# Optimization experiments

Hardware: AMD Instinct MI355X
Metric: run time of the kernel (lower is better)

The kernel has to match this reference:

```python
import jax, jax.numpy as jnp
import numpy as np

IMG = 32
CX = CY = IMG // 2
B = 65536


def setup_inputs() -> dict:
    key = jax.random.key(0)
    k1, k2, k3 = jax.random.split(key, 3)
    W = jax.random.normal(k1, (B, 16), dtype=jnp.float32)
    noise_randn = jax.random.normal(k2, (B, IMG, IMG), dtype=jnp.float32)
    noise_rand = jax.random.uniform(k3, (B, IMG, IMG), dtype=jnp.float32)
    return {"W": W, "noise_randn": noise_randn, "noise_rand": noise_rand}


def reference(W, noise_randn, noise_rand):
    H = IMG
    PI = jnp.float32(np.pi)
    ar = jnp.arange(H, dtype=jnp.float32)
    xx, yy = jnp.meshgrid(ar, ar, indexing="ij")  # (H, H)

    def c(k):  # per-sample scalar broadcast to (B,1,1)
        return W[:, k][:, None, None]

    r = jnp.sqrt((xx - CX) ** 2 + (yy - CY) ** 2)  # (H, H)

    # layer 0: clipped radial cone
    img = jnp.clip(c(0) * 5 - r, 0.0, 1.0)
    # layer 1: centered square (torch int(clamp(...).item()) == floor for positive vals)
    half = jnp.floor(jnp.clip(jnp.abs(c(1)) * 8, 2.0, 12.0))
    mask1 = ((xx >= CY - half) & (xx < CY + half) & (yy >= CX - half) & (yy < CX + half))
    img = img + 0.5 * mask1.astype(jnp.float32)
    # layers 2-4: sinusoids
    img = img + 0.5 * jnp.sin(c(2) * 10 * PI * xx / H)
    img = img + 0.5 * jnp.sin(c(3) * 10 * PI * yy / H)
    img = img + 0.5 * jnp.sin(c(4) * 5 * PI * (xx + yy) / (2 * H))
    # layer 5: warp
    img = img + 0.5 * jnp.sin((yy + c(5) * 10) * PI / H)
    # layer 6: bias
    img = img + c(6)
    # layer 7: gaussian blob; int() truncates toward zero
    bx = jnp.trunc(CX + c(7) * 5)
    by = jnp.trunc(CY + c(7) * 5)
    sigma = 4.0 + jnp.abs(c(7)) * 4.0
    img = img + jnp.exp(-((xx - bx) ** 2 + (yy - by) ** 2) / (2 * sigma ** 2))
    # layer 8: ring
    img = img + ((r - c(8) * 10) ** 2 < 10.0).astype(jnp.float32)
    # layer 9: checkerboard; cb_size = int(clamp(|w|*8+2, 2, 16)) -> floor
    cb = jnp.floor(jnp.clip(jnp.abs(c(9)) * 8 + 2, 2.0, 16.0))
    img = img + jnp.mod(jnp.floor(xx / cb) + jnp.floor(yy / cb), 2.0) * 0.3
    # layer 10: rotated line
    angle = c(10) * PI
    rot_line = jnp.cos(angle) * (xx - CX) + jnp.sin(angle) * (yy - CY)
    img = img + (jnp.abs(rot_line) < 3.0).astype(jnp.float32) * 0.6
    # layer 11: angular sinusoid
    theta = jnp.arctan2(yy - CY, xx - CX)
    img = img + 0.5 * jnp.sin(theta * c(11) * 5)
    # layers 12-13: noise (deterministic inputs replace randn_like/rand_like)
    img = img + noise_randn * 0.1 * c(12)
    img = img + (noise_rand - 0.5) * c(13) * 0.05
    # layer 14: contrast
    img = (img - 0.5) * (1.0 + c(14)) + 0.5
    # layer 15: conditional inversion
    img = jnp.where(c(15) > 0, 1.0 - img, img)
    # per-image min-max normalize
    mn = jnp.min(img, axis=(1, 2), keepdims=True)
    mx = jnp.max(img, axis=(1, 2), keepdims=True)
    img = (img - mn) / (mx - mn + 1e-8)
    return img[:, None, :, :]  # (B, 1, H, W)
```

## Files before the change

### kernel.cpp

```cpp
#include <hip/hip_runtime.h>
#include <math.h>

#define NB 65536
#define IMGD 32
#define NPIX 1024
#define PSTRIDE 20

__device__ float g_r[NPIX];
__device__ float g_th[NPIX];
__device__ float g_par[(size_t)NB * PSTRIDE];

__global__ void init_params_kernel(const float* __restrict__ W) {
    int b = blockIdx.x * blockDim.x + threadIdx.x;

    if (blockIdx.x == 0) {
        int t = threadIdx.x;
        for (int k = 0; k < 4; ++k) {
            int p = t * 4 + k;
            int x = p >> 5, y = p & 31;
            float dx = (float)(x - 16), dy = (float)(y - 16);
            g_r[p] = sqrtf(dx * dx + dy * dy);
            g_th[p] = atan2f(dy, dx) * 0.79577471545947668f;
        }
    }
    if (b >= NB) return;
    const float* w = W + (size_t)b * 16;
    float* P = g_par + (size_t)b * PSTRIDE;

    float w0 = w[0], w1 = w[1], w2 = w[2], w3 = w[3], w4 = w[4], w5 = w[5],
          w6 = w[6], w7 = w[7], w8 = w[8], w9 = w[9], w10 = w[10], w11 = w[11],
          w12 = w[12], w13 = w[13], w14 = w[14], w15 = w[15];

    P[0] = w0 * 5.0f;
    float half = floorf(fminf(fmaxf(fabsf(w1) * 8.0f, 2.0f), 12.0f));
    P[1] = 16.0f - half;
    P[2] = 16.0f + half;
    P[3] = w2 * 0.15625f;
    P[4] = w3 * 0.15625f;
    P[5] = w4 * 0.0390625f;
    P[6] = w5 * 0.15625f;
    P[7] = w6;
    float t7 = __fadd_rn(16.0f, __fmul_rn(w7, 5.0f));
    P[8] = truncf(t7);
    float sg = 4.0f + fabsf(w7) * 4.0f;
    P[9] = -1.0f / (2.0f * sg * sg);
    P[10] = w8 * 10.0f;
    float cb = floorf(fminf(fmaxf(__fadd_rn(fabsf(w9) * 8.0f, 2.0f), 2.0f), 16.0f));
    P[11] = cb;
    P[12] = 1.0f / cb;
    float ang = __fmul_rn(w10, 3.14159265358979323846f);
    P[13] = (float)cos((double)ang);
    P[14] = (float)sin((double)ang);
    P[15] = w11;
    P[16] = w12 * 0.1f;
    P[17] = w13 * 0.05f;
    P[18] = 1.0f + w14;
    P[19] = w15;
}

__device__ __forceinline__ float hsin(float rev) {
    rev = rev - floorf(rev);
    return __builtin_amdgcn_sinf(rev);
}

__device__ __forceinline__ float fdivq(float xf, float cb, float rcb) {
    float q = floorf(xf * rcb);
    q += ((q + 1.0f) * cb <= xf) ? 1.0f : 0.0f;
    q -= ((q * cb) > xf) ? 1.0f : 0.0f;
    return q;
}

__global__ __launch_bounds__(256) void decode_kernel(
        const float* __restrict__ nrand,
        const float* __restrict__ nunif,
        float* __restrict__ out) {
    int b = blockIdx.x;
    int t = threadIdx.x;
    const float* P = g_par + (size_t)b * PSTRIDE;

    float a0  = P[0],  lo  = P[1],  hi  = P[2],  s2  = P[3],  s3 = P[4];
    float s4  = P[5],  s5o = P[6],  w6  = P[7],  bxy = P[8],  nk = P[9];
    float t8  = P[10], cb  = P[11], rcb = P[12], ca  = P[13], sa = P[14];
    float w11 = P[15], k12 = P[16], k13 = P[17], con = P[18], w15 = P[19];

    __shared__ float4 xt4[32];
    __shared__ float4 yt4[36];
    __shared__ float  stab[63];

    if (t < 32) {
        float xf = (float)t;
        float qx = fdivq(xf, cb, rcb);
        float px = qx - 2.0f * floorf(qx * 0.5f);
        float d  = xf - bxy;
        float4 e;
        e.x = 0.5f * hsin(s2 * xf) + 0.3f * px;
        e.y = (xf >= lo && xf < hi) ? 1.0f : 0.0f;
        e.z = -0.6f * px;
        e.w = __expf(d * d * nk);
        xt4[t] = e;
    } else if (t < 64) {
        int   y  = t - 32;
        float yf = (float)y;
        float qy = fdivq(yf, cb, rcb);
        float py = qy - 2.0f * floorf(qy * 0.5f);
        float d  = yf - bxy;
        float4 e;
        e.x = 0.5f * hsin(s3 * yf) + 0.5f * hsin(0.015625f * yf + s5o)
              + 0.3f * py + w6;
        e.y = (yf >= lo && yf < hi) ? 0.5f : 0.0f;
        e.z = py;
        e.w = __expf(d * d * nk);
        yt4[y + (y >> 3)] = e;
    } else if (t < 127) {
        int s = t - 64;
        stab[s] = 0.5f * hsin(s4 * (float)s);
    }
    __syncthreads();

    int   y   = t & 31;
    int   x0  = t >> 5;
    float4 Y  = yt4[y + (y >> 3)];
    float yf  = (float)y;
    float sy  = __fmul_rn(sa, yf - 16.0f);

    size_t base = (size_t)b * NPIX + (size_t)t;
    const float* nrp = nrand + base;
    const float* nup = nunif + base;
    const float* rp  = g_r + t;
    const float* tp  = g_th + t;

    float img[4];
    float mn = 1e30f, mx = -1e30f;

#pragma unroll
    for (int j = 0; j < 4; ++j) {
        int   x  = x0 + 8 * j;
        float xf = (float)x;
        float r  = rp[256 * j];
        float4 X = xt4[x];

        float v = fminf(fmaxf(a0 - r, 0.0f), 1.0f);
        v += X.x + Y.x;
        v = fmaf(X.y, Y.y, v);
        v += stab[x + y];
        v = fmaf(X.z, Y.z, v);
        v = fmaf(X.w, Y.w, v);
        float dr = __fsub_rn(r, t8);
        v += (__fmul_rn(dr, dr) < 10.0f) ? 1.0f : 0.0f;
        float rot = __fadd_rn(__fmul_rn(ca, xf - 16.0f), sy);
        v += (fabsf(rot) < 3.0f) ? 0.6f : 0.0f;
        v += 0.5f * hsin(tp[256 * j] * w11);
        v = fmaf(nrp[256 * j], k12, v);
        v = fmaf(nup[256 * j] - 0.5f, k13, v);

        img[j] = v;
        mn = fminf(mn, v);
        mx = fmaxf(mx, v);
    }

#pragma unroll
    for (int off = 32; off > 0; off >>= 1) {
        mn = fminf(mn, __shfl_xor(mn, off));
        mx = fmaxf(mx, __shfl_xor(mx, off));
    }
    __shared__ float smn[4], smx[4];
    int wid = t >> 6;
    if ((t & 63) == 0) { smn[wid] = mn; smx[wid] = mx; }
    __syncthreads();
    mn = fminf(fminf(smn[0], smn[1]), fminf(smn[2], smn[3]));
    mx = fmaxf(fmaxf(smx[0], smx[1]), fmaxf(smx[2], smx[3]));

    float ac    = fabsf(con);
    float denom = fmaf(ac, mx - mn, 1e-8f);
    float s     = ac / denom;
    bool  eff   = (w15 > 0.0f) != (con < 0.0f);
    float bse   = eff ? mx : mn;
    float sgn   = eff ? -s : s;

    float* op = out + base;
#pragma unroll
    for (int j = 0; j < 4; ++j)
        op[256 * j] = (img[j] - bse) * sgn;
}

extern "C" void kernel_launch(void* const* d_in, const int* in_sizes, int n_in,
                              void* d_out, int out_size, void* d_ws, size_t ws_size,
                              hipStream_t stream) {
    const float* W  = (const float*)d_in[0];
    const float* nr = (const float*)d_in[1];
    const float* nu = (const float*)d_in[2];
    float* out = (float*)d_out;

    init_params_kernel<<<NB / 256, 256, 0, stream>>>(W);
    decode_kernel<<<NB, 256, 0, stream>>>(nr, nu, out);
}
```

Measured before the change: 147.2 us.

## Vectorize pixel loads/stores to float4 and pack math with v_pk_fma_f32

```diff
diff --git a/kernel.cpp b/kernel.cpp
--- a/kernel.cpp
+++ b/kernel.cpp
@@ -6,9 +6,24 @@
 #define NPIX 1024
 #define PSTRIDE 20
 
-__device__ float g_r[NPIX];
-__device__ float g_th[NPIX];
-__device__ float g_par[(size_t)NB * PSTRIDE];
+typedef float v2f __attribute__((ext_vector_type(2)));
+
+#define PK_FMA(d, a, b, c) \
+    asm("v_pk_fma_f32 %0, %1, %2, %3" : "=v"(d) : "v"(a), "v"(b), "v"(c))
+#define PK_FMA_CLAMP(d, a, b, c) \
+    asm("v_pk_fma_f32 %0, %1, %2, %3 clamp" : "=v"(d) : "v"(a), "v"(b), "v"(c))
+#define PK_FMA_ACC(acc, a, b) \
+    asm("v_pk_fma_f32 %0, %1, %2, %0" : "+v"(acc) : "v"(a), "v"(b))
+#define PK_ADD(d, a, b) \
+    asm("v_pk_add_f32 %0, %1, %2" : "=v"(d) : "v"(a), "v"(b))
+#define PK_ADD_ACC(acc, a) \
+    asm("v_pk_add_f32 %0, %0, %1" : "+v"(acc) : "v"(a))
+#define PK_MUL(d, a, b) \
+    asm("v_pk_mul_f32 %0, %1, %2" : "=v"(d) : "v"(a), "v"(b))
+
+__device__ __align__(16) float g_r[NPIX];
+__device__ __align__(16) float g_th[NPIX];
+__device__ __align__(16) float g_par[(size_t)NB * PSTRIDE];
 
 __global__ void init_params_kernel(const float* __restrict__ W) {
     int b = blockIdx.x * blockDim.x + threadIdx.x;
@@ -59,8 +74,7 @@
 }
 
 __device__ __forceinline__ float hsin(float rev) {
-    rev = rev - floorf(rev);
-    return __builtin_amdgcn_sinf(rev);
+    return __builtin_amdgcn_sinf(__builtin_amdgcn_fractf(rev));
 }
 
 __device__ __forceinline__ float fdivq(float xf, float cb, float rcb) {
@@ -76,15 +90,22 @@
         float* __restrict__ out) {
     int b = blockIdx.x;
     int t = threadIdx.x;
-    const float* P = g_par + (size_t)b * PSTRIDE;
-
-    float a0  = P[0],  lo  = P[1],  hi  = P[2],  s2  = P[3],  s3 = P[4];
-    float s4  = P[5],  s5o = P[6],  w6  = P[7],  bxy = P[8],  nk = P[9];
-    float t8  = P[10], cb  = P[11], rcb = P[12], ca  = P[13], sa = P[14];
-    float w11 = P[15], k12 = P[16], k13 = P[17], con = P[18], w15 = P[19];
+
+    const float4* Pq = (const float4*)(g_par + (size_t)b * PSTRIDE);
+    float4 q0 = Pq[0], q1 = Pq[1], q2 = Pq[2], q3 = Pq[3], q4 = Pq[4];
+    float a0 = q0.x, lo = q0.y, hi = q0.z, s2 = q0.w;
+    float s3 = q1.x, s4 = q1.y, s5o = q1.z, w6 = q1.w;
+    float bxy = q2.x, nk = q2.y, t8 = q2.z, cb = q2.w;
+    float rcb = q3.x, ca = q3.y, sa = q3.z, w11 = q3.w;
+    float k12 = q4.x, k13 = q4.y, con = q4.z, w15 = q4.w;
 
     __shared__ float4 xt4[32];
-    __shared__ float4 yt4[36];
+    __shared__ float  rx[32];
+    __shared__ float  ysum[32];
+    __shared__ float  ym05[32];
+    __shared__ float  pyt[32];
+    __shared__ float  gyt[32];
+    __shared__ float  syt[32];
     __shared__ float  stab[63];
 
     if (t < 32) {
@@ -98,64 +119,97 @@
         e.z = -0.6f * px;
         e.w = __expf(d * d * nk);
         xt4[t] = e;
+        rx[t] = __fmul_rn(ca, xf - 16.0f);
     } else if (t < 64) {
         int   y  = t - 32;
         float yf = (float)y;
         float qy = fdivq(yf, cb, rcb);
         float py = qy - 2.0f * floorf(qy * 0.5f);
         float d  = yf - bxy;
-        float4 e;
-        e.x = 0.5f * hsin(s3 * yf) + 0.5f * hsin(0.015625f * yf + s5o)
-              + 0.3f * py + w6;
-        e.y = (yf >= lo && yf < hi) ? 0.5f : 0.0f;
-        e.z = py;
-        e.w = __expf(d * d * nk);
-        yt4[y + (y >> 3)] = e;
+        ysum[y] = 0.5f * hsin(s3 * yf) + 0.5f * hsin(0.015625f * yf + s5o)
+                  + 0.3f * py + w6 - 0.5f * k13;
+        ym05[y] = (yf >= lo && yf < hi) ? 0.5f : 0.0f;
+        pyt[y]  = py;
+        gyt[y]  = __expf(d * d * nk);
+        syt[y]  = __fmul_rn(sa, yf - 16.0f);
     } else if (t < 127) {
         int s = t - 64;
         stab[s] = 0.5f * hsin(s4 * (float)s);
     }
     __syncthreads();
 
-    int   y   = t & 31;
-    int   x0  = t >> 5;
-    float4 Y  = yt4[y + (y >> 3)];
-    float yf  = (float)y;
-    float sy  = __fmul_rn(sa, yf - 16.0f);
-
-    size_t base = (size_t)b * NPIX + (size_t)t;
-    const float* nrp = nrand + base;
-    const float* nup = nunif + base;
-    const float* rp  = g_r + t;
-    const float* tp  = g_th + t;
-
-    float img[4];
-    float mn = 1e30f, mx = -1e30f;
+    int x  = t >> 3;
+    int y0 = (t & 7) * 4;
+
+    float4 X   = xt4[x];
+    float  rxv = rx[x];
+
+    v2f ysA = *(const v2f*)&ysum[y0], ysB = *(const v2f*)&ysum[y0 + 2];
+    v2f ymA = *(const v2f*)&ym05[y0], ymB = *(const v2f*)&ym05[y0 + 2];
+    v2f pyA = *(const v2f*)&pyt[y0],  pyB = *(const v2f*)&pyt[y0 + 2];
+    v2f gyA = *(const v2f*)&gyt[y0],  gyB = *(const v2f*)&gyt[y0 + 2];
+    v2f syA = *(const v2f*)&syt[y0],  syB = *(const v2f*)&syt[y0 + 2];
+    int s0 = x + y0;
+    v2f stA = {stab[s0], stab[s0 + 1]}, stB = {stab[s0 + 2], stab[s0 + 3]};
+
+    size_t q = (size_t)b * 256 + (size_t)t;
+    float4 R  = ((const float4*)g_r)[t];
+    float4 TH = ((const float4*)g_th)[t];
+    float4 NR = ((const float4*)nrand)[q];
+    float4 NU = ((const float4*)nunif)[q];
+
+    const v2f m1   = {-1.0f, -1.0f};
+    const v2f a02  = {a0, a0};
+    const v2f xs2  = {X.x, X.x};
+    const v2f xm2  = {X.y, X.y};
+    const v2f px2  = {X.z, X.z};
+    const v2f gx2  = {X.w, X.w};
+    const v2f rx2  = {rxv, rxv};
+    const v2f nt82 = {-t8, -t8};
+    const v2f w112 = {w11, w11};
+    const v2f h2   = {0.5f, 0.5f};
+    const v2f k122 = {k12, k12};
+    const v2f k132 = {k13, k13};
+
+    v2f i01, i23;
+    float mn, mx;
 
 #pragma unroll
-    for (int j = 0; j < 4; ++j) {
-        int   x  = x0 + 8 * j;
-        float xf = (float)x;
-        float r  = rp[256 * j];
-        float4 X = xt4[x];
-
-        float v = fminf(fmaxf(a0 - r, 0.0f), 1.0f);
-        v += X.x + Y.x;
-        v = fmaf(X.y, Y.y, v);
-        v += stab[x + y];
-        v = fmaf(X.z, Y.z, v);
-        v = fmaf(X.w, Y.w, v);
-        float dr = __fsub_rn(r, t8);
-        v += (__fmul_rn(dr, dr) < 10.0f) ? 1.0f : 0.0f;
-        float rot = __fadd_rn(__fmul_rn(ca, xf - 16.0f), sy);
-        v += (fabsf(rot) < 3.0f) ? 0.6f : 0.0f;
-        v += 0.5f * hsin(tp[256 * j] * w11);
-        v = fmaf(nrp[256 * j], k12, v);
-        v = fmaf(nup[256 * j] - 0.5f, k13, v);
-
-        img[j] = v;
-        mn = fminf(mn, v);
-        mx = fmaxf(mx, v);
+    for (int k = 0; k < 2; ++k) {
+        v2f r2  = k ? (v2f){R.z, R.w}   : (v2f){R.x, R.y};
+        v2f th2 = k ? (v2f){TH.z, TH.w} : (v2f){TH.x, TH.y};
+        v2f nr2 = k ? (v2f){NR.z, NR.w} : (v2f){NR.x, NR.y};
+        v2f nu2 = k ? (v2f){NU.z, NU.w} : (v2f){NU.x, NU.y};
+        v2f ys = k ? ysB : ysA, ym = k ? ymB : ymA, py = k ? pyB : pyA;
+        v2f gy = k ? gyB : gyA, sy = k ? syB : syA, st = k ? stB : stA;
+
+        v2f v;
+        PK_FMA_CLAMP(v, r2, m1, a02);
+        PK_ADD_ACC(v, ys);
+        PK_ADD_ACC(v, xs2);
+        PK_ADD_ACC(v, st);
+        PK_FMA_ACC(v, xm2, ym);
+        PK_FMA_ACC(v, px2, py);
+        PK_FMA_ACC(v, gx2, gy);
+        v2f dr, dr2, rot, ang;
+        PK_ADD(dr, r2, nt82);
+        PK_MUL(dr2, dr, dr);
+        PK_ADD(rot, sy, rx2);
+        PK_MUL(ang, th2, w112);
+        v2f sn = {hsin(ang.x), hsin(ang.y)};
+        PK_FMA_ACC(v, sn, h2);
+        PK_FMA_ACC(v, nr2, k122);
+        PK_FMA_ACC(v, nu2, k132);
+
+        float vx = v.x + ((dr2.x < 10.0f) ? 1.0f : 0.0f);
+        float vy = v.y + ((dr2.y < 10.0f) ? 1.0f : 0.0f);
+        vx += (fabsf(rot.x) < 3.0f) ? 0.6f : 0.0f;
+        vy += (fabsf(rot.y) < 3.0f) ? 0.6f : 0.0f;
+
+        v2f r_ = {vx, vy};
+        if (k == 0) { i01 = r_; mn = fminf(vx, vy); mx = fmaxf(vx, vy); }
+        else        { i23 = r_; mn = fminf(mn, fminf(vx, vy));
+                                mx = fmaxf(mx, fmaxf(vx, vy)); }
     }
 
 #pragma unroll
@@ -176,11 +230,14 @@
     bool  eff   = (w15 > 0.0f) != (con < 0.0f);
     float bse   = eff ? mx : mn;
     float sgn   = eff ? -s : s;
-
-    float* op = out + base;
-#pragma unroll
-    for (int j = 0; j < 4; ++j)
-        op[256 * j] = (img[j] - bse) * sgn;
+    v2f c12 = {sgn, sgn};
+    v2f c02 = {-bse * sgn, -bse * sgn};
+
+    v2f o01, o23;
+    PK_FMA(o01, i01, c12, c02);
+    PK_FMA(o23, i23, c12, c02);
+    float4 O = {o01.x, o01.y, o23.x, o23.y};
+    ((float4*)out)[q] = O;
 }
 
 extern "C" void kernel_launch(void* const* d_in, const int* in_sizes, int n_in,
```

After: 152.6 us. +3.7%, slower.
